# Optimization experiments

Hardware: AMD Instinct MI355X
Metric: run time of the kernel (lower is better)

The kernel has to match this reference:

```python
import jax, jax.numpy as jnp
import numpy as np

N, G, HID, LAT, E_RAND = 20000, 3000, 256, 32, 320000
EPS = 1e-8
NEG_SLOPE = 0.2  # PyG GATv2Conv default leaky_relu slope


def _segment_softmax(logits, seg, n):
    # numerically stable softmax over edges grouped by destination node
    m = jax.ops.segment_max(logits, seg, num_segments=n)
    ex = jnp.exp(logits - m[seg])
    s = jax.ops.segment_sum(ex, seg, num_segments=n)
    return ex / (s[seg] + 1e-16)


def _gatv2(x, src, dst, Wl, Wr, att, b, n):
    # GATv2 (heads=1): score = att . leaky_relu(Wl x_j + Wr x_i)
    xl = x @ Wl  # [N, C] source transform (also the message)
    xr = x @ Wr  # [N, C] destination transform
    e = jax.nn.leaky_relu(xl[src] + xr[dst], NEG_SLOPE)  # [E, C]
    logit = e @ att  # [E]
    alpha = _segment_softmax(logit, dst, n)
    out = jax.ops.segment_sum(alpha[:, None] * xl[src], dst, num_segments=n)
    return out + b


def _log_zinb(x, mu, theta, pi):
    theta = theta[None, :]
    softplus_pi = jax.nn.softplus(-pi)
    log_theta_eps = jnp.log(theta + EPS)
    log_theta_mu_eps = jnp.log(theta + mu + EPS)
    pi_theta_log = -pi + theta * (log_theta_eps - log_theta_mu_eps)
    case_zero = jax.nn.softplus(pi_theta_log) - softplus_pi
    case_nz = (-softplus_pi + pi_theta_log
               + x * (jnp.log(mu + EPS) - log_theta_mu_eps)
               + jax.lax.lgamma(x + theta) - jax.lax.lgamma(theta)
               - jax.lax.lgamma(x + 1.0))
    return jnp.where(x < EPS, case_zero, 0.0) + jnp.where(x > EPS, case_nz, 0.0)


def setup_inputs():
    key = jax.random.key(0)
    ks = jax.random.split(key, 14)
    x = jax.random.randint(ks[0], (N, G), 0, 20).astype(jnp.float32)
    er = jax.random.randint(ks[1], (2, E_RAND), 0, N, dtype=jnp.int32)
    loops = jnp.tile(jnp.arange(N, dtype=jnp.int32)[None, :], (2, 1))
    edge_index = jnp.concatenate([er, loops], axis=1)  # [2, 340000] incl self-loops
    noise = jax.random.normal(ks[2], (N, LAT), dtype=jnp.float32)

    def init(k, shape, fan_in):
        return jax.random.normal(k, shape, dtype=jnp.float32) / np.float32(np.sqrt(fan_in))

    Wl1 = init(ks[3], (G, HID), G); Wr1 = init(ks[4], (G, HID), G)
    att1 = init(ks[5], (HID,), HID); b1 = jnp.zeros((HID,), jnp.float32)
    Wl2 = init(ks[6], (HID, 2 * LAT), HID); Wr2 = init(ks[7], (HID, 2 * LAT), HID)
    att2 = init(ks[8], (2 * LAT,), 2 * LAT); b2 = jnp.zeros((2 * LAT,), jnp.float32)
    Wd1 = init(ks[9], (LAT, HID), LAT); bd1 = jnp.zeros((HID,), jnp.float32)
    Wd2 = init(ks[10], (HID, G), HID); bd2 = jnp.zeros((G,), jnp.float32)
    Wdo = init(ks[11], (HID, G), HID); bdo = jnp.zeros((G,), jnp.float32)
    theta = jax.random.uniform(ks[12], (G,), minval=0.5, maxval=2.0, dtype=jnp.float32)
    return dict(x=x, edge_index=edge_index, noise=noise,
                Wl1=Wl1, Wr1=Wr1, att1=att1, b1=b1,
                Wl2=Wl2, Wr2=Wr2, att2=att2, b2=b2,
                Wd1=Wd1, bd1=bd1, Wd2=Wd2, bd2=bd2, Wdo=Wdo, bdo=bdo,
                theta=theta)


def reference(x, edge_index, noise, Wl1, Wr1, att1, b1, Wl2, Wr2, att2, b2,
              Wd1, bd1, Wd2, bd2, Wdo, bdo, theta):
    n = x.shape[0]
    src, dst = edge_index[0], edge_index[1]
    # --- GATv2 encoder ---
    h = _gatv2(x, src, dst, Wl1, Wr1, att1, b1, n)
    h2 = _gatv2(jax.nn.relu(h), src, dst, Wl2, Wr2, att2, b2, n)  # [N, 2*LAT]
    mu_z, logvar = h2[:, :LAT], h2[:, LAT:]
    # --- reparameterize: std = sqrt(exp(logvar)) ---
    z = mu_z + noise * jnp.exp(0.5 * logvar)
    # --- ZINB decoder ---
    hd = z @ Wd1 + bd1
    mean = jax.nn.softplus(hd @ Wd2 + bd2)
    pi = hd @ Wdo + bdo
    # --- loss: -E[log ZINB] + KL(q(z|x) || N(0,I)) ---
    recon = -jnp.mean(jnp.sum(_log_zinb(x, mean, theta, pi), axis=1))
    kl = jnp.mean(0.5 * jnp.sum(mu_z ** 2 + jnp.exp(logvar) - logvar - 1.0, axis=1))
    return recon + kl
```

## Files before the change

kernel.cpp:

```cpp
#include <hip/hip_runtime.h>
#include <math.h>

#define NN   20000
#define GG   3000
#define HIDD 256
#define LATT 32
#define FEPS 1e-8f

typedef __attribute__((ext_vector_type(8))) __bf16 bf16x8;
typedef __attribute__((ext_vector_type(4))) float f32x4;

__device__ __forceinline__ float fsp(float v) {
    float t = __expf(-fabsf(v));
    return fmaxf(v, 0.f) + __logf(1.f + t);
}
__device__ __forceinline__ float sp_approx(float t) {
    float a = fabsf(t);
    float den = fmaf(a, fmaf(a, fmaf(a, 0.8382f, -1.4958f), 1.87f), 1.f);
    return fmaxf(t, 0.f) + 0.6931472f * __builtin_amdgcn_rcpf(den);
}
__device__ __forceinline__ float lrelu(float v) {
    return v > 0.f ? v : 0.2f * v;
}
__device__ __forceinline__ ushort f2bf(float f) {
    uint b = __float_as_uint(f);
    return (ushort)((b + 0x7FFFu + ((b >> 16) & 1u)) >> 16);
}
__device__ __forceinline__ uint pk2(float a, float b) {
    return (uint)f2bf(a) | ((uint)f2bf(b) << 16);
}
__device__ __forceinline__ void gload16(const void* g, void* l) {
    __builtin_amdgcn_global_load_lds((const __attribute__((address_space(1))) void*)g,
                                     (__attribute__((address_space(3))) void*)l, 16, 0, 0);
}

__global__ void zinb_table(const float* __restrict__ theta, float* __restrict__ tabL,
                           float* __restrict__ logte, int G_) {
    int idx = blockIdx.x * blockDim.x + threadIdx.x;
    if (idx >= G_ * 20) return;
    int g = idx / 20, c = idx % 20;
    float th = theta[g];
    tabL[idx] = lgammaf((float)c + th) - lgammaf(th) - lgammaf((float)c + 1.f);
    if (c == 0) logte[g] = logf(th + FEPS);
}

__global__ void edge_hist(const int* __restrict__ ei, int* __restrict__ cnt, int E) {
    int e = blockIdx.x * blockDim.x + threadIdx.x;
    if (e < E) atomicAdd(&cnt[ei[E + e]], 1);
}

__global__ __launch_bounds__(1024)
void scan_deg(int* __restrict__ cnt_cur, int* __restrict__ rowptr, int Nn) {
    __shared__ int ts[1024];
    int t = threadIdx.x;
    int chunk = (Nn + 1023) / 1024;
    int beg = t * chunk, end = min(beg + chunk, Nn);
    int s = 0;
    for (int i = beg; i < end; i++) s += cnt_cur[i];
    ts[t] = s;
    __syncthreads();
    for (int off = 1; off < 1024; off <<= 1) {
        int v = (t >= off) ? ts[t - off] : 0;
        __syncthreads();
        ts[t] += v;
        __syncthreads();
    }
    int run = (t == 0) ? 0 : ts[t - 1];
    for (int i = beg; i < end; i++) {
        int c = cnt_cur[i];
        rowptr[i] = run;
        cnt_cur[i] = run;
        run += c;
    }
    if (t == 1023) rowptr[Nn] = ts[1023];
}

__global__ void edge_scatter(const int* __restrict__ ei, int* __restrict__ cur,
                             int* __restrict__ eidx, int E) {
    int e = blockIdx.x * blockDim.x + threadIdx.x;
    if (e < E) {
        int p = atomicAdd(&cur[ei[E + e]], 1);
        eidx[p] = e;
    }
}

__global__ __launch_bounds__(256)
void transp_bf16(const float* __restrict__ in, ushort* __restrict__ out,
                 int K, int N, int Kpad) {
    __shared__ ushort t[32][33];
    int k0 = blockIdx.x * 32, n0 = blockIdx.y * 32;
    int tx = threadIdx.x & 31, ty = threadIdx.x >> 5;
    #pragma unroll
    for (int u = 0; u < 32; u += 8) {
        int k = k0 + ty + u, n = n0 + tx;
        t[ty + u][tx] = (k < K && n < N) ? f2bf(in[(size_t)k * N + n]) : (ushort)0;
    }
    __syncthreads();
    #pragma unroll
    for (int u = 0; u < 32; u += 8) {
        int n = n0 + ty + u, k = k0 + tx;
        if (n < N && k < Kpad) out[(size_t)n * Kpad + k] = t[tx][ty + u];
    }
}

__global__ __launch_bounds__(256)
void wcomb(const float* __restrict__ Wd1, const float* __restrict__ bd1,
           const float* __restrict__ Wd2, const float* __restrict__ bd2,
           const float* __restrict__ Wdo, const float* __restrict__ bdo,
           ushort* __restrict__ W2t, ushort* __restrict__ Wot,
           float* __restrict__ b2c, float* __restrict__ boc, int G_) {
    __shared__ float w1s[32 * 256];
    int tid = threadIdx.x;
    for (int i = tid; i < 32 * 256; i += 256) w1s[i] = Wd1[i];
    __syncthreads();
    int gl = tid & 63, rg = tid >> 6;
    int g = blockIdx.x * 64 + gl;
    int gc = min(g, G_ - 1);
    float a2[8], ao[8];
    #pragma unroll
    for (int i = 0; i < 8; i++) { a2[i] = 0.f; ao[i] = 0.f; }
    float ab2 = 0.f, abo = 0.f;
    for (int j = 0; j < 256; j++) {
        float w2 = Wd2[(size_t)j * G_ + gc];
        float wo = Wdo[(size_t)j * G_ + gc];
        if (rg == 0) {
            float b1 = bd1[j];
            ab2 = fmaf(b1, w2, ab2);
            abo = fmaf(b1, wo, abo);
        }
        #pragma unroll
        for (int i = 0; i < 8; i++) {
            float w1 = w1s[(rg * 8 + i) * 256 + j];
            a2[i] = fmaf(w1, w2, a2[i]);
            ao[i] = fmaf(w1, wo, ao[i]);
        }
    }
    if (g < G_) {
        #pragma unroll
        for (int i = 0; i < 8; i++) {
            W2t[(size_t)g * 32 + rg * 8 + i] = f2bf(a2[i]);
            Wot[(size_t)g * 32 + rg * 8 + i] = f2bf(ao[i]);
        }
        if (rg == 0) { b2c[g] = ab2 + bd2[g]; boc[g] = abo + bdo[g]; }
    }
}

__global__ __launch_bounds__(256, 4)
void dec_zinb(const ushort* __restrict__ zb, const ushort* __restrict__ W2t,
              const ushort* __restrict__ Wot, const float* __restrict__ xg,
              const float* __restrict__ tabL, const float* __restrict__ theta,
              const float* __restrict__ logte, const float* __restrict__ b2c,
              const float* __restrict__ boc, double* __restrict__ partsR,
              int M, int G_) {
    __shared__ float tabs[64 * 20];
    __shared__ float thetas[64], thltes[64], bd2s[64], bdos[64];
    __shared__ double redd[4];
    const int tid = threadIdx.x;
    const int nwg = gridDim.x * gridDim.y;
    const int orig = blockIdx.y * gridDim.x + blockIdx.x;
    const int q = nwg >> 3, r = nwg & 7, xcd = orig & 7;
    const int vv = (xcd < r ? xcd * (q + 1) : r * (q + 1) + (xcd - r) * q) + (orig >> 3);
    const int bx = vv % gridDim.x, by = vv / gridDim.x;
    const int m0 = by * 128, n0 = bx * 64;
    const int lane = tid & 63, wid = tid >> 6;
    const int wr = wid >> 1, wc = wid & 1;
    const int frow = lane & 15;
    const int ksl = (lane >> 4) << 3;

    for (int i = tid; i < 64; i += 256) {
        int g = n0 + i;
        bool ok = g < G_;
        float th = ok ? theta[g] : 1.f;
        thetas[i] = th;
        thltes[i] = ok ? th * logte[g] : 0.f;
        bd2s[i]   = ok ? b2c[g] : 0.f;
        bdos[i]   = ok ? boc[g] : 0.f;
    }
    for (int i = tid; i < 64 * 20; i += 256) {
        int g = n0 + i / 20;
        tabs[i] = (g < G_) ? tabL[(size_t)g * 20 + i % 20] : 0.f;
    }

    f32x4 acc1[4][2], acc2[4][2];
    #pragma unroll
    for (int i = 0; i < 4; i++)
        #pragma unroll
        for (int j = 0; j < 2; j++) {
            acc1[i][j] = (f32x4){0.f, 0.f, 0.f, 0.f};
            acc2[i][j] = (f32x4){0.f, 0.f, 0.f, 0.f};
        }

    bf16x8 af[4];
    #pragma unroll
    for (int mi = 0; mi < 4; mi++) {
        int gm = min(m0 + (wr << 6) + (mi << 4) + frow, M - 1);
        af[mi] = *(const bf16x8*)(zb + (size_t)gm * 32 + ksl);
    }
    #pragma unroll
    for (int ni = 0; ni < 2; ni++) {
        int gn = min(n0 + (wc << 5) + (ni << 4) + frow, G_ - 1);
        bf16x8 bf1 = *(const bf16x8*)(W2t + (size_t)gn * 32 + ksl);
        bf16x8 bf2 = *(const bf16x8*)(Wot + (size_t)gn * 32 + ksl);
        #pragma unroll
        for (int mi = 0; mi < 4; mi++) {
            acc1[mi][ni] = __builtin_amdgcn_mfma_f32_16x16x32_bf16(af[mi], bf1, acc1[mi][ni], 0, 0, 0);
            acc2[mi][ni] = __builtin_amdgcn_mfma_f32_16x16x32_bf16(af[mi], bf2, acc2[mi][ni], 0, 0, 0);
        }
    }
    __syncthreads();

    const int lr = (lane >> 4) << 2;
    float lsum = 0.f;
    #pragma unroll
    for (int mi = 0; mi < 4; mi++)
        #pragma unroll
        for (int ni = 0; ni < 2; ni++) {
            int lcol = (wc << 5) + (ni << 4) + frow;
            int gn = n0 + lcol;
            int gmb = m0 + (wr << 6) + (mi << 4) + lr;
            if (gn >= G_) continue;
            float xv4[4];
            #pragma unroll
            for (int j = 0; j < 4; j++) {
                int gm = min(gmb + j, M - 1);
                xv4[j] = xg[(size_t)gm * G_ + gn];
            }
            f32x4 am = acc1[mi][ni], ap = acc2[mi][ni];
            float th = thetas[lcol], thlte = thltes[lcol];
            float bm = bd2s[lcol], bp = bdos[lcol];
            #pragma unroll
            for (int j = 0; j < 4; j++) {
                if (gmb + j >= M) continue;
                float mu  = fsp(am[j] + bm);
                float pi  = ap[j] + bp;
                float spp = fsp(pi);
                float ltme = __logf(th + mu + FEPS);
                float lmu  = __logf(mu + FEPS);
                float xv = xv4[j];
                int xi = (int)(xv + 0.5f);
                float ptl = fmaf(-th, ltme, thlte) - pi;
                float corr = (xv < FEPS) ? sp_approx(-ptl) : 0.f;
                lsum += thlte + tabs[lcol * 20 + xi] - spp
                      - (th + xv) * ltme + xv * lmu + corr;
            }
        }
    #pragma unroll
    for (int off = 32; off; off >>= 1) lsum += __shfl_down(lsum, off);
    if (lane == 0) redd[wid] = (double)lsum;
    __syncthreads();
    if (tid == 0)
        partsR[by * gridDim.x + bx] = redd[0] + redd[1] + redd[2] + redd[3];
}

__global__ __launch_bounds__(512, 1)
void gemm_big(const float* __restrict__ Ap, const ushort* __restrict__ B1t,
              const ushort* __restrict__ B2t, float* __restrict__ C1,
              float* __restrict__ C2, int M, int Kreal, int Kpad, int Nc) {
    __shared__ __align__(16) char lds[98304];

    const int tid = threadIdx.x;
    const int nwg = gridDim.x * gridDim.y;
    const int orig = blockIdx.y * gridDim.x + blockIdx.x;
    const int q = nwg >> 3, r = nwg & 7, xcd = orig & 7;
    const int vv = (xcd < r ? xcd * (q + 1) : r * (q + 1) + (xcd - r) * q) + (orig >> 3);
    const int bx = vv % gridDim.x, by = vv / gridDim.x;
    const int m0 = by * 128, n0 = bx * 128;
    const int lane = tid & 63, wid = tid >> 6;
    const int wr = wid >> 2, wc = wid & 3;
    const int frow = lane & 15;
    const int fkb = (lane >> 4) << 4;

    const int row_in = lane >> 3;
    const int sch = (lane & 7) ^ (row_in & 7);
    const int ldso = (lane << 4);
    const int arow = tid >> 2;
    const int acol = (tid & 3) << 4;
    const int ao0 = ((arow << 7) + (acol << 1)) ^ ((arow & 7) << 4);
    const int ao1 = ((arow << 7) + ((acol + 8) << 1)) ^ ((arow & 7) << 4);
    const int gmA = min(m0 + arow, M - 1);
    const float* arowp = Ap + (size_t)gmA * Kreal;

    f32x4 acc1[4][2], acc2[4][2];
    #pragma unroll
    for (int i = 0; i < 4; i++)
        #pragma unroll
        for (int j = 0; j < 2; j++) {
            acc1[i][j] = (f32x4){0.f, 0.f, 0.f, 0.f};
            acc2[i][j] = (f32x4){0.f, 0.f, 0.f, 0.f};
        }

    auto stageB = [&](int k0, char* dB1, char* dB2) {
        #pragma unroll
        for (int u = 0; u < 2; u++) {
            int s = (wid << 1) + u;
            int grow = n0 + (s << 3) + row_in;
            if (grow > Nc - 1) grow = Nc - 1;
            size_t go = (size_t)grow * Kpad + k0 + (sch << 3);
            gload16(B1t + go, dB1 + (s << 10) + ldso);
            gload16(B2t + go, dB2 + (s << 10) + ldso);
        }
    };
    auto loadA = [&](int k0, float* av) {
        if (k0 + 64 <= Kreal) {
            const float* af = arowp + k0 + acol;
            float4 a = ((const float4*)af)[0];
            float4 b = ((const float4*)af)[1];
            float4 c = ((const float4*)af)[2];
            float4 d = ((const float4*)af)[3];
            av[0]=a.x; av[1]=a.y; av[2]=a.z; av[3]=a.w;
            av[4]=b.x; av[5]=b.y; av[6]=b.z; av[7]=b.w;
            av[8]=c.x; av[9]=c.y; av[10]=c.z; av[11]=c.w;
            av[12]=d.x; av[13]=d.y; av[14]=d.z; av[15]=d.w;
        } else {
            #pragma unroll
            for (int jj = 0; jj < 16; jj++) {
                int gk = k0 + acol + jj;
                av[jj] = (gk < Kreal) ? arowp[gk] : 0.f;
            }
        }
    };
    auto writeA = [&](const float* av, char* dA) {
        uint4 w0, w1;
        w0.x = pk2(av[0], av[1]);   w0.y = pk2(av[2], av[3]);
        w0.z = pk2(av[4], av[5]);   w0.w = pk2(av[6], av[7]);
        w1.x = pk2(av[8], av[9]);   w1.y = pk2(av[10], av[11]);
        w1.z = pk2(av[12], av[13]); w1.w = pk2(av[14], av[15]);
        *(uint4*)(dA + ao0) = w0;
        *(uint4*)(dA + ao1) = w1;
    };

    const int nk = Kpad >> 6;
    {
        stageB(0, lds + 16384, lds + 32768);
        float av[16];
        loadA(0, av);
        writeA(av, lds);
    }
    __syncthreads();

    for (int t = 0; t < nk; t++) {
        char* cbuf = lds + ((t & 1) ? 49152 : 0);
        char* nbuf = lds + ((t & 1) ? 0 : 49152);
        float av[16];
        const bool more = (t + 1 < nk);
        if (more) {
            stageB((t + 1) << 6, nbuf + 16384, nbuf + 32768);
            loadA((t + 1) << 6, av);
        }
        char* ldsA  = cbuf;
        char* ldsB1 = cbuf + 16384;
        char* ldsB2 = cbuf + 32768;
        #pragma unroll
        for (int kk = 0; kk < 2; kk++) {
            int kb = (kk << 6) + fkb;
            bf16x8 af[4], b1f[2], b2f[2];
            #pragma unroll
            for (int mi = 0; mi < 4; mi++) {
                int rr = (wr << 6) + (mi << 4) + frow;
                int o = ((rr << 7) + kb) ^ ((rr & 7) << 4);
                af[mi] = *(const bf16x8*)(ldsA + o);
            }
            #pragma unroll
            for (int ni = 0; ni < 2; ni++) {
                int rr = (wc << 5) + (ni << 4) + frow;
                int o = ((rr << 7) + kb) ^ ((rr & 7) << 4);
                b1f[ni] = *(const bf16x8*)(ldsB1 + o);
                b2f[ni] = *(const bf16x8*)(ldsB2 + o);
            }
            #pragma unroll
            for (int mi = 0; mi < 4; mi++)
                #pragma unroll
                for (int ni = 0; ni < 2; ni++) {
                    acc1[mi][ni] = __builtin_amdgcn_mfma_f32_16x16x32_bf16(af[mi], b1f[ni], acc1[mi][ni], 0, 0, 0);
                    acc2[mi][ni] = __builtin_amdgcn_mfma_f32_16x16x32_bf16(af[mi], b2f[ni], acc2[mi][ni], 0, 0, 0);
                }
        }
        if (more) writeA(av, nbuf);
        __syncthreads();
    }

    const int lr = (lane >> 4) << 2;
    #pragma unroll
    for (int mi = 0; mi < 4; mi++)
        #pragma unroll
        for (int ni = 0; ni < 2; ni++) {
            int gmb = m0 + (wr << 6) + (mi << 4) + lr;
            int gn  = n0 + (wc << 5) + (ni << 4) + frow;
            if (gn >= Nc) continue;
            f32x4 v1 = acc1[mi][ni], v2 = acc2[mi][ni];
            #pragma unroll
            for (int j = 0; j < 4; j++) {
                int gm = gmb + j;
                if (gm < M) {
                    C1[(size_t)gm * Nc + gn] = v1[j];
                    C2[(size_t)gm * Nc + gn] = v2[j];
                }
            }
        }
}

__global__ __launch_bounds__(256, 4)
void mfma_dual(const void* __restrict__ Ap, const ushort* __restrict__ B1t,
               const ushort* __restrict__ B2t, float* __restrict__ C1,
               float* __restrict__ C2, int M, int K, int Nc) {
    __shared__ __align__(16) char lds[24576];
    char* ldsA  = lds;
    char* ldsB1 = lds + 8192;
    char* ldsB2 = lds + 16384;

    const int tid = threadIdx.x;
    const int m0 = blockIdx.y * 64, n0 = blockIdx.x * 64;
    const int lane = tid & 63, wid = tid >> 6;
    const int wr = wid >> 1, wc = wid & 1;
    const int frow = lane & 15;
    const int fkb = (lane >> 4) << 4;

    f32x4 acc1[2][2], acc2[2][2];
    #pragma unroll
    for (int i = 0; i < 2; i++)
        #pragma unroll
        for (int j = 0; j < 2; j++) {
            acc1[i][j] = (f32x4){0.f, 0.f, 0.f, 0.f};
            acc2[i][j] = (f32x4){0.f, 0.f, 0.f, 0.f};
        }

    const int nk = (K + 63) >> 6;
    for (int t = 0; t < nk; t++) {
        const int k0 = t << 6;
        #pragma unroll
        for (int u = 0; u < 2; u++) {
            int c = tid + (u << 8);
            int row = c >> 3, col8 = (c & 7) << 3;
            int gm = m0 + row, gk = k0 + col8;
            uint4 w = make_uint4(0u, 0u, 0u, 0u);
            if (gm < M && gk < K)
                w = *(const uint4*)((const ushort*)Ap + (size_t)gm * K + gk);
            int o = ((row << 7) + (col8 << 1)) ^ ((row & 7) << 4);
            *(uint4*)(ldsA + o) = w;
        }
        #pragma unroll
        for (int u = 0; u < 2; u++) {
            int c = tid + (u << 8);
            int row = c >> 3, col8 = (c & 7) << 3;
            int gn = n0 + row, gk = k0 + col8;
            uint4 w1 = make_uint4(0u, 0u, 0u, 0u), w2 = w1;
            if (gn < Nc && gk < K) {
                size_t o = (size_t)gn * K + gk;
                w1 = *(const uint4*)(B1t + o);
                w2 = *(const uint4*)(B2t + o);
            }
            int o = ((row << 7) + (col8 << 1)) ^ ((row & 7) << 4);
            *(uint4*)(ldsB1 + o) = w1;
            *(uint4*)(ldsB2 + o) = w2;
        }
        __syncthreads();
        #pragma unroll
        for (int kk = 0; kk < 2; kk++) {
            int kb = (kk << 6) + fkb;
            bf16x8 af[2], b1f[2], b2f[2];
            #pragma unroll
            for (int mi = 0; mi < 2; mi++) {
                int rr = (wr << 5) + (mi << 4) + frow;
                int o = ((rr << 7) + kb) ^ ((rr & 7) << 4);
                af[mi] = *(const bf16x8*)(ldsA + o);
            }
            #pragma unroll
            for (int ni = 0; ni < 2; ni++) {
                int rr = (wc << 5) + (ni << 4) + frow;
                int o = ((rr << 7) + kb) ^ ((rr & 7) << 4);
                b1f[ni] = *(const bf16x8*)(ldsB1 + o);
                b2f[ni] = *(const bf16x8*)(ldsB2 + o);
            }
            #pragma unroll
            for (int mi = 0; mi < 2; mi++)
                #pragma unroll
                for (int ni = 0; ni < 2; ni++) {
                    acc1[mi][ni] = __builtin_amdgcn_mfma_f32_16x16x32_bf16(af[mi], b1f[ni], acc1[mi][ni], 0, 0, 0);
                    acc2[mi][ni] = __builtin_amdgcn_mfma_f32_16x16x32_bf16(af[mi], b2f[ni], acc2[mi][ni], 0, 0, 0);
                }
        }
        __syncthreads();
    }

    const int lr = (lane >> 4) << 2;
    #pragma unroll
    for (int mi = 0; mi < 2; mi++)
        #pragma unroll
        for (int ni = 0; ni < 2; ni++) {
            int gmb = m0 + (wr << 5) + (mi << 4) + lr;
            int gn  = n0 + (wc << 5) + (ni << 4) + frow;
            if (gn >= Nc) continue;
            f32x4 v1 = acc1[mi][ni], v2 = acc2[mi][ni];
            #pragma unroll
            for (int j = 0; j < 4; j++) {
                int gm = gmb + j;
                if (gm < M) {
                    C1[(size_t)gm * Nc + gn] = v1[j];
                    C2[(size_t)gm * Nc + gn] = v2[j];
                }
            }
        }
}

template<int DW, int OM>
__global__ __launch_bounds__(256)
void gat_attn(const float* __restrict__ xl, const float* __restrict__ xr,
              const float* __restrict__ att, const int* __restrict__ ei,
              const int* __restrict__ rowptr, const int* __restrict__ eidx,
              const float* __restrict__ bias, void* __restrict__ out,
              int D, int Nn) {
    int wid = threadIdx.x >> 6, lane = threadIdx.x & 63;
    int n = blockIdx.x * 4 + wid;
    if (n >= Nn) return;
    int k = lane * DW;
    float xrr[DW], ats[DW], hacc[DW];
    if (DW == 4) {
        float4 a4 = *(const float4*)(att + k);
        float4 r4 = *(const float4*)(xr + (size_t)n * D + k);
        ats[0] = a4.x; ats[1] = a4.y; ats[2] = a4.z; ats[3] = a4.w;
        xrr[0] = r4.x; xrr[1] = r4.y; xrr[2] = r4.z; xrr[3] = r4.w;
    } else {
        ats[0] = att[k];
        xrr[0] = xr[(size_t)n * D + k];
    }
    #pragma unroll
    for (int d = 0; d < DW; d++) hacc[d] = 0.f;
    float m = -3.0e38f, ssum = 0.f;
    int beg = rowptr[n], end = rowptr[n + 1];
    for (int j = beg; j < end; j++) {
        int e = eidx[j];
        const float* xs = xl + (size_t)ei[e] * D + k;
        float v[DW];
        float p;
        if (DW == 4) {
            float4 v4 = *(const float4*)xs;
            v[0] = v4.x; v[1] = v4.y; v[2] = v4.z; v[3] = v4.w;
            p = ats[0] * lrelu(v[0] + xrr[0]) + ats[1] * lrelu(v[1] + xrr[1])
              + ats[2] * lrelu(v[2] + xrr[2]) + ats[3] * lrelu(v[3] + xrr[3]);
        } else {
            v[0] = xs[0];
            p = ats[0] * lrelu(v[0] + xrr[0]);
        }
        #pragma unroll
        for (int o2 = 32; o2; o2 >>= 1) p += __shfl_xor(p, o2);
        float mnew = fmaxf(m, p);
        float sc = __expf(m - mnew);
        float w  = __expf(p - mnew);
        ssum = fmaf(ssum, sc, w);
        #pragma unroll
        for (int d = 0; d < DW; d++) hacc[d] = fmaf(hacc[d], sc, w * v[d]);
        m = mnew;
    }
    float inv = 1.f / (ssum + 1e-16f);
    if (DW == 4) {
        float4 b = *(const float4*)(bias + k);
        float r0 = fmaf(hacc[0], inv, b.x), r1 = fmaf(hacc[1], inv, b.y);
        float r2 = fmaf(hacc[2], inv, b.z), r3 = fmaf(hacc[3], inv, b.w);
        if (OM == 0) {
            *(float4*)((float*)out + (size_t)n * D + k) = make_float4(r0, r1, r2, r3);
        } else {
            ushort4 o;
            o.x = f2bf(fmaxf(r0, 0.f)); o.y = f2bf(fmaxf(r1, 0.f));
            o.z = f2bf(fmaxf(r2, 0.f)); o.w = f2bf(fmaxf(r3, 0.f));
            *(ushort4*)((ushort*)out + (size_t)n * D + k) = o;
        }
    } else {
        float r0 = fmaf(hacc[0], inv, bias[k]);
        if (OM == 0) ((float*)out)[(size_t)n * D + k] = r0;
        else         ((ushort*)out)[(size_t)n * D + k] = f2bf(fmaxf(r0, 0.f));
    }
}

__global__ __launch_bounds__(256)
void z_kl(const float* __restrict__ h2, const float* __restrict__ noise,
          ushort* __restrict__ z, double* __restrict__ partsK, int Nn) {
    __shared__ double rd[4];
    int gid = blockIdx.x * blockDim.x + threadIdx.x;
    int n = gid >> 5, k = gid & 31;
    float kt = 0.f;
    if (n < Nn) {
        float mu = h2[(size_t)n * 64 + k];
        float lv = h2[(size_t)n * 64 + 32 + k];
        float ev = expf(lv);
        z[(size_t)n * 32 + k] = f2bf(mu + noise[(size_t)n * 32 + k] * expf(0.5f * lv));
        kt = 0.5f * (mu * mu + ev - lv - 1.f);
    }
    #pragma unroll
    for (int off = 32; off; off >>= 1) kt += __shfl_down(kt, off);
    int wid = threadIdx.x >> 6, lane = threadIdx.x & 63;
    if (lane == 0) rd[wid] = (double)kt;
    __syncthreads();
    if (threadIdx.x == 0) partsK[blockIdx.x] = rd[0] + rd[1] + rd[2] + rd[3];
}

__global__ __launch_bounds__(256)
void final_reduce(const double* __restrict__ pR, int nR,
                  const double* __restrict__ pK, int nK,
                  float* __restrict__ out, int Nn) {
    __shared__ double sd[256];
    double s = 0.0;
    for (int i = threadIdx.x; i < nR; i += 256) s -= pR[i];
    for (int i = threadIdx.x; i < nK; i += 256) s += pK[i];
    sd[threadIdx.x] = s;
    __syncthreads();
    for (int o = 128; o; o >>= 1) {
        if (threadIdx.x < o) sd[threadIdx.x] += sd[threadIdx.x + o];
        __syncthreads();
    }
    if (threadIdx.x == 0) out[0] = (float)(sd[0] / (double)Nn);
}

extern "C" void kernel_launch(void* const* d_in, const int* in_sizes, int n_in,
                              void* d_out, int out_size, void* d_ws, size_t ws_size,
                              hipStream_t stream) {
    const int N_ = NN, G_ = GG, HID_ = HIDD;
    const int KP1 = 3008;
    const float* x     = (const float*)d_in[0];
    const int*   ei    = (const int*)d_in[1];
    const float* noise = (const float*)d_in[2];
    const float* Wl1   = (const float*)d_in[3];
    const float* Wr1   = (const float*)d_in[4];
    const float* att1  = (const float*)d_in[5];
    const float* b1    = (const float*)d_in[6];
    const float* Wl2   = (const float*)d_in[7];
    const float* Wr2   = (const float*)d_in[8];
    const float* att2  = (const float*)d_in[9];
    const float* b2    = (const float*)d_in[10];
    const float* Wd1   = (const float*)d_in[11];
    const float* bd1   = (const float*)d_in[12];
    const float* Wd2   = (const float*)d_in[13];
    const float* bd2   = (const float*)d_in[14];
    const float* Wdo   = (const float*)d_in[15];
    const float* bdo   = (const float*)d_in[16];
    const float* theta = (const float*)d_in[17];
    const int E = in_sizes[1] / 2;

    const int MB128 = (N_ + 127) / 128;
    const int DGX   = (G_ + 63) / 64;
    const int nR    = DGX * MB128;
    const int nKb   = (N_ * 32) / 256;

    char* base = (char*)d_ws;
    size_t off = 0;
    auto alloc = [&](size_t bytes) -> char* {
        char* p = base + off;
        off = (off + bytes + 255) & ~(size_t)255;
        return p;
    };
    double* partsR = (double*)alloc((size_t)nR * 8);
    double* partsK = (double*)alloc((size_t)nKb * 8);
    float*  tabL  = (float*)alloc((size_t)G_ * 20 * 4);
    float*  logte = (float*)alloc((size_t)G_ * 4);
    int*    rowptr= (int*)alloc((size_t)(N_ + 1) * 4);
    int*    cur   = (int*)alloc((size_t)N_ * 4);
    int*    eidx  = (int*)alloc((size_t)E * 4);
    ushort* Wl1t  = (ushort*)alloc((size_t)HID_ * KP1 * 2);
    ushort* Wr1t  = (ushort*)alloc((size_t)HID_ * KP1 * 2);
    ushort* Wl2t  = (ushort*)alloc((size_t)64 * HID_ * 2);
    ushort* Wr2t  = (ushort*)alloc((size_t)64 * HID_ * 2);
    ushort* W2t   = (ushort*)alloc((size_t)G_ * 32 * 2);
    ushort* Wot   = (ushort*)alloc((size_t)G_ * 32 * 2);
    float*  b2c   = (float*)alloc((size_t)G_ * 4);
    float*  boc   = (float*)alloc((size_t)G_ * 4);
    float*  xl1   = (float*)alloc((size_t)N_ * HID_ * 4);
    float*  xr1   = (float*)alloc((size_t)N_ * HID_ * 4);
    ushort* h_bf  = (ushort*)alloc((size_t)N_ * HID_ * 2);
    float*  xl2   = (float*)alloc((size_t)N_ * 64 * 4);
    float*  xr2   = (float*)alloc((size_t)N_ * 64 * 4);
    float*  h2    = (float*)alloc((size_t)N_ * 64 * 4);
    ushort* zb    = (ushort*)alloc((size_t)N_ * 32 * 2);

    float*  outf = (float*)d_out;

    hipMemsetAsync(cur, 0, N_ * sizeof(int), stream);

    zinb_table<<<(G_ * 20 + 255) / 256, 256, 0, stream>>>(theta, tabL, logte, G_);
    edge_hist<<<(E + 255) / 256, 256, 0, stream>>>(ei, cur, E);
    scan_deg<<<1, 1024, 0, stream>>>(cur, rowptr, N_);
    edge_scatter<<<(E + 255) / 256, 256, 0, stream>>>(ei, cur, eidx, E);

    transp_bf16<<<dim3(KP1 / 32, (HID_ + 31) / 32), 256, 0, stream>>>(Wl1, Wl1t, G_, HID_, KP1);
    transp_bf16<<<dim3(KP1 / 32, (HID_ + 31) / 32), 256, 0, stream>>>(Wr1, Wr1t, G_, HID_, KP1);
    transp_bf16<<<dim3(HID_ / 32, 2), 256, 0, stream>>>(Wl2, Wl2t, HID_, 64, HID_);
    transp_bf16<<<dim3(HID_ / 32, 2), 256, 0, stream>>>(Wr2, Wr2t, HID_, 64, HID_);

    wcomb<<<(G_ + 63) / 64, 256, 0, stream>>>(
        Wd1, bd1, Wd2, bd2, Wdo, bdo, W2t, Wot, b2c, boc, G_);

    gemm_big<<<dim3(HID_ / 128, MB128), 512, 0, stream>>>(
        x, Wl1t, Wr1t, xl1, xr1, N_, G_, KP1, HID_);
    gat_attn<4, 1><<<(N_ + 3) / 4, 256, 0, stream>>>(
        xl1, xr1, att1, ei, rowptr, eidx, b1, h_bf, HID_, N_);

    mfma_dual<<<dim3(1, (N_ + 63) / 64), 256, 0, stream>>>(
        h_bf, Wl2t, Wr2t, xl2, xr2, N_, HID_, 64);
    gat_attn<1, 0><<<(N_ + 3) / 4, 256, 0, stream>>>(
        xl2, xr2, att2, ei, rowptr, eidx, b2, h2, 64, N_);

    z_kl<<<nKb, 256, 0, stream>>>(h2, noise, zb, partsK, N_);

    dec_zinb<<<dim3(DGX, MB128), 256, 0, stream>>>(
        zb, W2t, Wot, x, tabL, theta, logte, b2c, boc, partsR, N_, G_);

    final_reduce<<<1, 256, 0, stream>>>(partsR, nR, partsK, nKb, outf, N_);
}
```

Measured before the change: 640.1 us.

## Pre-convert x to bf16 and carry layer-1 GAT features in bf16

```diff
diff --git a/kernel.cpp b/kernel.cpp
--- a/kernel.cpp
+++ b/kernel.cpp
@@ -5,6 +5,7 @@
 #define GG   3000
 #define HIDD 256
 #define LATT 32
+#define KP1  3008
 #define FEPS 1e-8f
 
 typedef __attribute__((ext_vector_type(8))) __bf16 bf16x8;
@@ -26,12 +27,31 @@
     uint b = __float_as_uint(f);
     return (ushort)((b + 0x7FFFu + ((b >> 16) & 1u)) >> 16);
 }
+__device__ __forceinline__ float bf2f(ushort u) {
+    return __uint_as_float((uint)u << 16);
+}
 __device__ __forceinline__ uint pk2(float a, float b) {
     return (uint)f2bf(a) | ((uint)f2bf(b) << 16);
 }
 __device__ __forceinline__ void gload16(const void* g, void* l) {
     __builtin_amdgcn_global_load_lds((const __attribute__((address_space(1))) void*)g,
                                      (__attribute__((address_space(3))) void*)l, 16, 0, 0);
+}
+
+__global__ __launch_bounds__(256)
+void x2bf(const float* __restrict__ x, ushort* __restrict__ xb) {
+    const size_t nch = (size_t)NN * (GG / 8);
+    size_t i = (size_t)blockIdx.x * 256 + threadIdx.x;
+    if (i >= nch) return;
+    size_t row = i / (GG / 8);
+    int c8 = (int)(i % (GG / 8)) * 8;
+    const float* p = x + row * GG + c8;
+    float4 a = ((const float4*)p)[0];
+    float4 b = ((const float4*)p)[1];
+    uint4 w;
+    w.x = pk2(a.x, a.y); w.y = pk2(a.z, a.w);
+    w.z = pk2(b.x, b.y); w.w = pk2(b.z, b.w);
+    *(uint4*)(xb + row * GG + c8) = w;
 }
 
 __global__ void zinb_table(const float* __restrict__ theta, float* __restrict__ tabL,
@@ -147,7 +167,7 @@
 
 __global__ __launch_bounds__(256, 4)
 void dec_zinb(const ushort* __restrict__ zb, const ushort* __restrict__ W2t,
-              const ushort* __restrict__ Wot, const float* __restrict__ xg,
+              const ushort* __restrict__ Wot, const ushort* __restrict__ xb,
               const float* __restrict__ tabL, const float* __restrict__ theta,
               const float* __restrict__ logte, const float* __restrict__ b2c,
               const float* __restrict__ boc, double* __restrict__ partsR,
@@ -223,7 +243,7 @@
             #pragma unroll
             for (int j = 0; j < 4; j++) {
                 int gm = min(gmb + j, M - 1);
-                xv4[j] = xg[(size_t)gm * G_ + gn];
+                xv4[j] = bf2f(xb[(size_t)gm * G_ + gn]);
             }
             f32x4 am = acc1[mi][ni], ap = acc2[mi][ni];
             float th = thetas[lcol], thlte = thltes[lcol];
@@ -252,11 +272,14 @@
         partsR[by * gridDim.x + bx] = redd[0] + redd[1] + redd[2] + redd[3];
 }
 
-__global__ __launch_bounds__(512, 1)
-void gemm_big(const float* __restrict__ Ap, const ushort* __restrict__ B1t,
-              const ushort* __restrict__ B2t, float* __restrict__ C1,
-              float* __restrict__ C2, int M, int Kreal, int Kpad, int Nc) {
-    __shared__ __align__(16) char lds[98304];
+__global__ __launch_bounds__(512, 4)
+void gemm_big(const ushort* __restrict__ At, const ushort* __restrict__ B1t,
+              const ushort* __restrict__ B2t, ushort* __restrict__ C1,
+              ushort* __restrict__ C2, int M, int Ka, int Kpad, int Nc) {
+    __shared__ __align__(16) char lds[49152];
+    char* ldsA  = lds;
+    char* ldsB1 = lds + 16384;
+    char* ldsB2 = lds + 32768;
 
     const int tid = threadIdx.x;
     const int nwg = gridDim.x * gridDim.y;
@@ -273,12 +296,6 @@
     const int row_in = lane >> 3;
     const int sch = (lane & 7) ^ (row_in & 7);
     const int ldso = (lane << 4);
-    const int arow = tid >> 2;
-    const int acol = (tid & 3) << 4;
-    const int ao0 = ((arow << 7) + (acol << 1)) ^ ((arow & 7) << 4);
-    const int ao1 = ((arow << 7) + ((acol + 8) << 1)) ^ ((arow & 7) << 4);
-    const int gmA = min(m0 + arow, M - 1);
-    const float* arowp = Ap + (size_t)gmA * Kreal;
 
     f32x4 acc1[4][2], acc2[4][2];
     #pragma unroll
@@ -289,67 +306,22 @@
             acc2[i][j] = (f32x4){0.f, 0.f, 0.f, 0.f};
         }
 
-    auto stageB = [&](int k0, char* dB1, char* dB2) {
+    const int nk = Kpad >> 6;
+    for (int t = 0; t < nk; t++) {
+        const int k0 = t << 6;
         #pragma unroll
         for (int u = 0; u < 2; u++) {
             int s = (wid << 1) + u;
-            int grow = n0 + (s << 3) + row_in;
-            if (grow > Nc - 1) grow = Nc - 1;
-            size_t go = (size_t)grow * Kpad + k0 + (sch << 3);
-            gload16(B1t + go, dB1 + (s << 10) + ldso);
-            gload16(B2t + go, dB2 + (s << 10) + ldso);
-        }
-    };
-    auto loadA = [&](int k0, float* av) {
-        if (k0 + 64 <= Kreal) {
-            const float* af = arowp + k0 + acol;
-            float4 a = ((const float4*)af)[0];
-            float4 b = ((const float4*)af)[1];
-            float4 c = ((const float4*)af)[2];
-            float4 d = ((const float4*)af)[3];
-            av[0]=a.x; av[1]=a.y; av[2]=a.z; av[3]=a.w;
-            av[4]=b.x; av[5]=b.y; av[6]=b.z; av[7]=b.w;
-            av[8]=c.x; av[9]=c.y; av[10]=c.z; av[11]=c.w;
-            av[12]=d.x; av[13]=d.y; av[14]=d.z; av[15]=d.w;
-        } else {
-            #pragma unroll
-            for (int jj = 0; jj < 16; jj++) {
-                int gk = k0 + acol + jj;
-                av[jj] = (gk < Kreal) ? arowp[gk] : 0.f;
-            }
-        }
-    };
-    auto writeA = [&](const float* av, char* dA) {
-        uint4 w0, w1;
-        w0.x = pk2(av[0], av[1]);   w0.y = pk2(av[2], av[3]);
-        w0.z = pk2(av[4], av[5]);   w0.w = pk2(av[6], av[7]);
-        w1.x = pk2(av[8], av[9]);   w1.y = pk2(av[10], av[11]);
-        w1.z = pk2(av[12], av[13]); w1.w = pk2(av[14], av[15]);
-        *(uint4*)(dA + ao0) = w0;
-        *(uint4*)(dA + ao1) = w1;
-    };
-
-    const int nk = Kpad >> 6;
-    {
-        stageB(0, lds + 16384, lds + 32768);
-        float av[16];
-        loadA(0, av);
-        writeA(av, lds);
-    }
-    __syncthreads();
-
-    for (int t = 0; t < nk; t++) {
-        char* cbuf = lds + ((t & 1) ? 49152 : 0);
-        char* nbuf = lds + ((t & 1) ? 0 : 49152);
-        float av[16];
-        const bool more = (t + 1 < nk);
-        if (more) {
-            stageB((t + 1) << 6, nbuf + 16384, nbuf + 32768);
-            loadA((t + 1) << 6, av);
-        }
-        char* ldsA  = cbuf;
-        char* ldsB1 = cbuf + 16384;
-        char* ldsB2 = cbuf + 32768;
+            int gnb = n0 + (s << 3) + row_in;
+            size_t gob = (size_t)gnb * Kpad + k0 + (sch << 3);
+            gload16(B1t + gob, ldsB1 + (s << 10) + ldso);
+            gload16(B2t + gob, ldsB2 + (s << 10) + ldso);
+            int gma = m0 + (s << 3) + row_in;
+            if (gma > M - 1) gma = M - 1;
+            size_t goa = (size_t)gma * Ka + k0 + (sch << 3);
+            gload16(At + goa, ldsA + (s << 10) + ldso);
+        }
+        __syncthreads();
         #pragma unroll
         for (int kk = 0; kk < 2; kk++) {
             int kb = (kk << 6) + fkb;
@@ -375,7 +347,6 @@
                     acc2[mi][ni] = __builtin_amdgcn_mfma_f32_16x16x32_bf16(af[mi], b2f[ni], acc2[mi][ni], 0, 0, 0);
                 }
         }
-        if (more) writeA(av, nbuf);
         __syncthreads();
     }
 
@@ -392,8 +363,8 @@
             for (int j = 0; j < 4; j++) {
                 int gm = gmb + j;
                 if (gm < M) {
-                    C1[(size_t)gm * Nc + gn] = v1[j];
-                    C2[(size_t)gm * Nc + gn] = v2[j];
+                    C1[(size_t)gm * Nc + gn] = f2bf(v1[j]);
+                    C2[(size_t)gm * Nc + gn] = f2bf(v2[j]);
                 }
             }
         }
@@ -502,9 +473,9 @@
         }
 }
 
-template<int DW, int OM>
+template<int DW, int OM, int IBF>
 __global__ __launch_bounds__(256)
-void gat_attn(const float* __restrict__ xl, const float* __restrict__ xr,
+void gat_attn(const void* __restrict__ xlv, const void* __restrict__ xrv,
               const float* __restrict__ att, const int* __restrict__ ei,
               const int* __restrict__ rowptr, const int* __restrict__ eidx,
               const float* __restrict__ bias, void* __restrict__ out,
@@ -516,12 +487,18 @@
     float xrr[DW], ats[DW], hacc[DW];
     if (DW == 4) {
         float4 a4 = *(const float4*)(att + k);
-        float4 r4 = *(const float4*)(xr + (size_t)n * D + k);
         ats[0] = a4.x; ats[1] = a4.y; ats[2] = a4.z; ats[3] = a4.w;
-        xrr[0] = r4.x; xrr[1] = r4.y; xrr[2] = r4.z; xrr[3] = r4.w;
+        if (IBF) {
+            ushort4 u = *(const ushort4*)((const ushort*)xrv + (size_t)n * D + k);
+            xrr[0] = bf2f(u.x); xrr[1] = bf2f(u.y); xrr[2] = bf2f(u.z); xrr[3] = bf2f(u.w);
+        } else {
+            float4 r4 = *(const float4*)((const float*)xrv + (size_t)n * D + k);
+            xrr[0] = r4.x; xrr[1] = r4.y; xrr[2] = r4.z; xrr[3] = r4.w;
+        }
     } else {
         ats[0] = att[k];
-        xrr[0] = xr[(size_t)n * D + k];
+        xrr[0] = IBF ? bf2f(((const ushort*)xrv)[(size_t)n * D + k])
+                     : ((const float*)xrv)[(size_t)n * D + k];
     }
     #pragma unroll
     for (int d = 0; d < DW; d++) hacc[d] = 0.f;
@@ -529,16 +506,22 @@
     int beg = rowptr[n], end = rowptr[n + 1];
     for (int j = beg; j < end; j++) {
         int e = eidx[j];
-        const float* xs = xl + (size_t)ei[e] * D + k;
+        int src = ei[e];
         float v[DW];
         float p;
         if (DW == 4) {
-            float4 v4 = *(const float4*)xs;
-            v[0] = v4.x; v[1] = v4.y; v[2] = v4.z; v[3] = v4.w;
+            if (IBF) {
+                ushort4 u = *(const ushort4*)((const ushort*)xlv + (size_t)src * D + k);
+                v[0] = bf2f(u.x); v[1] = bf2f(u.y); v[2] = bf2f(u.z); v[3] = bf2f(u.w);
+            } else {
+                float4 v4 = *(const float4*)((const float*)xlv + (size_t)src * D + k);
+                v[0] = v4.x; v[1] = v4.y; v[2] = v4.z; v[3] = v4.w;
+            }
             p = ats[0] * lrelu(v[0] + xrr[0]) + ats[1] * lrelu(v[1] + xrr[1])
               + ats[2] * lrelu(v[2] + xrr[2]) + ats[3] * lrelu(v[3] + xrr[3]);
         } else {
-            v[0] = xs[0];
+            v[0] = IBF ? bf2f(((const ushort*)xlv)[(size_t)src * D + k])
+                       : ((const float*)xlv)[(size_t)src * D + k];
             p = ats[0] * lrelu(v[0] + xrr[0]);
         }
         #pragma unroll
@@ -614,7 +597,6 @@
                               void* d_out, int out_size, void* d_ws, size_t ws_size,
                               hipStream_t stream) {
     const int N_ = NN, G_ = GG, HID_ = HIDD;
-    const int KP1 = 3008;
     const float* x     = (const float*)d_in[0];
     const int*   ei    = (const int*)d_in[1];
     const float* noise = (const float*)d_in[2];
@@ -662,18 +644,20 @@
     ushort* Wot   = (ushort*)alloc((size_t)G_ * 32 * 2);
     float*  b2c   = (float*)alloc((size_t)G_ * 4);
     float*  boc   = (float*)alloc((size_t)G_ * 4);
-    float*  xl1   = (float*)alloc((size_t)N_ * HID_ * 4);
-    float*  xr1   = (float*)alloc((size_t)N_ * HID_ * 4);
+    ushort* xb    = (ushort*)alloc((size_t)N_ * G_ * 2);
+    ushort* xl1b  = (ushort*)alloc((size_t)N_ * HID_ * 2);
+    ushort* xr1b  = (ushort*)alloc((size_t)N_ * HID_ * 2);
     ushort* h_bf  = (ushort*)alloc((size_t)N_ * HID_ * 2);
-    float*  xl2   = (float*)alloc((size_t)N_ * 64 * 4);
-    float*  xr2   = (float*)alloc((size_t)N_ * 64 * 4);
-    float*  h2    = (float*)alloc((size_t)N_ * 64 * 4);
-    ushort* zb    = (ushort*)alloc((size_t)N_ * 32 * 2);
+    float*  xl2 = (float*)xl1b;
+    float*  xr2 = xl2 + (size_t)N_ * 64;
+    float*  h2  = xr2 + (size_t)N_ * 64;
+    ushort* zb  = (ushort*)(h2 + (size_t)N_ * 64);
 
     float*  outf = (float*)d_out;
 
     hipMemsetAsync(cur, 0, N_ * sizeof(int), stream);
 
+    x2bf<<<(int)(((size_t)N_ * (G_ / 8) + 255) / 256), 256, 0, stream>>>(x, xb);
     zinb_table<<<(G_ * 20 + 255) / 256, 256, 0, stream>>>(theta, tabL, logte, G_);
     edge_hist<<<(E + 255) / 256, 256, 0, stream>>>(ei, cur, E);
     scan_deg<<<1, 1024, 0, stream>>>(cur, rowptr, N_);
@@ -688,19 +672,19 @@
         Wd1, bd1, Wd2, bd2, Wdo, bdo, W2t, Wot, b2c, boc, G_);
 
     gemm_big<<<dim3(HID_ / 128, MB128), 512, 0, stream>>>(
-        x, Wl1t, Wr1t, xl1, xr1, N_, G_, KP1, HID_);
-    gat_attn<4, 1><<<(N_ + 3) / 4, 256, 0, stream>>>(
-        xl1, xr1, att1, ei, rowptr, eidx, b1, h_bf, HID_, N_);
+        xb, Wl1t, Wr1t, xl1b, xr1b, N_, G_, KP1, HID_);
+    gat_attn<4, 1, 1><<<(N_ + 3) / 4, 256, 0, stream>>>(
+        xl1b, xr1b, att1, ei, rowptr, eidx, b1, h_bf, HID_, N_);
 
     mfma_dual<<<dim3(1, (N_ + 63) / 64), 256, 0, stream>>>(
         h_bf, Wl2t, Wr2t, xl2, xr2, N_, HID_, 64);
-    gat_attn<1, 0><<<(N_ + 3) / 4, 256, 0, stream>>>(
+    gat_attn<1, 0, 0><<<(N_ + 3) / 4, 256, 0, stream>>>(
         xl2, xr2, att2, ei, rowptr, eidx, b2, h2, 64, N_);
 
     z_kl<<<nKb, 256, 0, stream>>>(h2, noise, zb, partsK, N_);
 
     dec_zinb<<<dim3(DGX, MB128), 256, 0, stream>>>(
-        zb, W2t, Wot, x, tabL, theta, logte, b2c, boc, partsR, N_, G_);
+        zb, W2t, Wot, xb, tabL, theta, logte, b2c, boc, partsR, N_, G_);
 
     final_reduce<<<1, 256, 0, stream>>>(partsR, nR, partsK, nKb, outf, N_);
 }
```

After: 630.9 us. About the same (-1.4%).
